# Optimization experiments

Measured on AMD Instinct MI355X. Metric: run time of the kernel, lower is better.

## Reference

```python
import jax, jax.numpy as jnp
import numpy as np

KS = 3  # kernel_size
NH, HD = 16, 64
EPS = 1e-5

# fixed offset grid v: [27, 3], meshgrid 'ij' of [-1,0,1]
_offs = np.arange(-(KS // 2), KS // 2 + 1)
V_GRID = jnp.asarray(np.stack(np.meshgrid(_offs, _offs, _offs, indexing='ij'), -1).reshape(KS ** 3, 3), dtype=jnp.float32)


def setup_inputs() -> dict:
    key = jax.random.key(0)
    ks = jax.random.split(key, 8)
    B, Cf, Cm, H, W, T = 1, 64, 64, 32, 32, 32
    C = NH * HD
    inp = {
        'F': jax.random.normal(ks[0], (B, Cf, H, W, T), jnp.float32),
        'M': jax.random.normal(ks[1], (B, Cm, H, W, T), jnp.float32),
        'gamma_f': jnp.ones((Cf,), jnp.float32),
        'beta_f': jnp.zeros((Cf,), jnp.float32),
        'w_f': jax.random.normal(ks[2], (Cf, C), jnp.float32) * 0.05,
        'b_f': jnp.zeros((C,), jnp.float32),
        'gamma_m': jnp.ones((Cm,), jnp.float32),
        'beta_m': jnp.zeros((Cm,), jnp.float32),
        'w_m': jax.random.normal(ks[3], (Cm, C), jnp.float32) * 0.05,
        'b_m': jnp.zeros((C,), jnp.float32),
        'rpb': jax.random.normal(ks[4], (NH, KS, KS, KS), jnp.float32) * 0.02,
    }
    return inp


def _pe(x, gamma, beta, w, b):
    # permute to channels-last, LayerNorm over channels, Linear proj
    x = jnp.transpose(x, (0, 2, 3, 4, 1))  # [B,H,W,T,Cin]
    mu = jnp.mean(x, axis=-1, keepdims=True)
    var = jnp.mean((x - mu) ** 2, axis=-1, keepdims=True)
    x = (x - mu) / jnp.sqrt(var + EPS) * gamma + beta
    return x @ w + b  # [B,H,W,T,C]


def _mdt_forward(F, M, gamma_f, beta_f, w_f, b_f, gamma_m, beta_m, w_m, b_m, rpb):
    scale = 1.0  # qk_scale=1
    q = _pe(F, gamma_f, beta_f, w_f, b_f)
    k = _pe(M, gamma_m, beta_m, w_m, b_m)
    B, H, W, T, C = q.shape
    nh, hd = NH, C // NH
    # [B,nh,H,W,T,hd]
    q = jnp.transpose(q.reshape(B, H, W, T, nh, hd), (0, 4, 1, 2, 3, 5)) * scale
    k = jnp.transpose(k.reshape(B, H, W, T, nh, hd), (0, 4, 1, 2, 3, 5))
    pdr = (KS - 1) // 2
    kp = jnp.pad(k, ((0, 0), (0, 0), (pdr, pdr), (pdr, pdr), (pdr, pdr), (0, 0)))
    # 3x3x3 neighborhood qk: attn [B,nh,H,W,T,27], neighbor order = dz*9+dy*3+dx (matches rpb/v flatten)
    scores = [
        jnp.einsum('bnhwtd,bnhwtd->bnhwt', q,
                   jax.lax.dynamic_slice(kp, (0, 0, dz, dy, dx, 0), (B, nh, H, W, T, hd)))
        for dz in range(KS) for dy in range(KS) for dx in range(KS)
    ]
    attn = jnp.stack(scores, axis=-1) + rpb.reshape(nh, KS ** 3)[None, :, None, None, None, :]
    attn = jax.nn.softmax(attn, axis=-1)
    x = jnp.einsum('bnhwtk,kc->bnhwtc', attn, V_GRID)  # [B,nh,H,W,T,3]
    x = jnp.transpose(x, (0, 1, 5, 2, 3, 4)).reshape(B, nh * 3, H, W, T)
    return x


def reference(F, M, gamma_f, beta_f, w_f, b_f, gamma_m, beta_m, w_m, b_m, rpb):
    return _mdt_forward(F, M, gamma_f, beta_f, w_f, b_f, gamma_m, beta_m, w_m, b_m, rpb)
```

## Files before the change

### kernel.cpp

```cpp
#include <hip/hip_runtime.h>
#include <hip/hip_bf16.h>
#include <cstdint>
#include <cstddef>

#define NVOX   32768
#define CIN    64
#define COUT   1024
#define NHEAD  16
#define HD     64
#define EPSV   1e-5f
#define MT     128
#define ROWP   72
#define OBP    136
#define KCP    72
#define KCOLS  2304
#define SCP    28

using bf16x8 = __attribute__((ext_vector_type(8))) short;
using f32x4  = __attribute__((ext_vector_type(4))) float;

__device__ __forceinline__ float bf2f(unsigned short h) {
    union { unsigned u; float f; } x; x.u = ((unsigned)h) << 16; return x.f;
}
__device__ __forceinline__ unsigned short f2bf(float f) {
    __hip_bfloat16 h = __float2bfloat16(f);
    return *reinterpret_cast<unsigned short*>(&h);
}
__device__ __forceinline__ unsigned packbf2(float a, float b) {
    return (unsigned)f2bf(a) | ((unsigned)f2bf(b) << 16);
}
template<bool BF>
__device__ __forceinline__ float LD(const void* p, size_t i) {
    if constexpr (BF) return bf2f(((const unsigned short*)p)[i]);
    else              return ((const float*)p)[i];
}
__device__ __forceinline__ int is_bf(const void* gf) {
    return ((const unsigned*)gf)[0] == 0x3F803F80u;
}

__global__ __launch_bounds__(256) void wtrans_kernel(
    const void* __restrict__ w_f, const void* __restrict__ w_m,
    const void* __restrict__ gf,
    unsigned short* __restrict__ wTf, unsigned short* __restrict__ wTm)
{
    const int bfq = is_bf(gf);
    const int sel = blockIdx.x >> 8;
    const void* w = sel ? w_m : w_f;
    unsigned short* wT = sel ? wTm : wTf;
    const int b = blockIdx.x & 255;
    const int t = threadIdx.x;
    const int c = t & 63, nl = t >> 6;
    const int n = b * 4 + nl;
    const float v = bfq ? bf2f(((const unsigned short*)w)[(size_t)c * COUT + n])
                        : ((const float*)w)[(size_t)c * COUT + n];
    wT[(size_t)n * CIN + c] = f2bf(v);
}

template<bool BF>
__device__ __forceinline__ void proj_body(
    const void* __restrict__ X,
    const void* __restrict__ gamma,
    const void* __restrict__ beta,
    const unsigned short* __restrict__ wT,
    const void* __restrict__ bias,
    unsigned short* __restrict__ out,
    char* smem)
{
    unsigned short* xnT = (unsigned short*)smem;
    unsigned short* ob  = (unsigned short*)(smem + 18432);
    float* bl           = (float*)(smem + 18432 + 17408);

    const int tid = threadIdx.x;
    const int vbase = blockIdx.x * MT;
    const int jbase = blockIdx.y * 128;
    const int wv = tid >> 6;
    const int lane = tid & 63;
    const int mm = lane & 15;
    const int quad = lane >> 4;

    if (tid < 128) bl[tid] = LD<BF>(bias, jbase + tid);

    bf16x8 bfrag[2][2];
    #pragma unroll
    for (int nt = 0; nt < 2; ++nt) {
        const int jg = jbase + wv * 32 + nt * 16 + mm;
        #pragma unroll
        for (int s = 0; s < 2; ++s)
            bfrag[nt][s] = *reinterpret_cast<const bf16x8*>(wT + (size_t)jg * CIN + s * 32 + quad * 8);
    }

    {
        const int v = tid >> 1, hf = tid & 1;
        float vals[32];
        #pragma unroll
        for (int c = 0; c < 32; ++c)
            vals[c] = LD<BF>(X, (size_t)(hf * 32 + c) * NVOX + vbase + v);
        float s = 0.f;
        #pragma unroll
        for (int c = 0; c < 32; ++c) s += vals[c];
        s += __shfl_xor(s, 1);
        const float mu = s * (1.f / 64.f);
        float var = 0.f;
        #pragma unroll
        for (int c = 0; c < 32; ++c) { const float d = vals[c] - mu; var += d * d; }
        var += __shfl_xor(var, 1);
        const float rs = rsqrtf(var * (1.f / 64.f) + EPSV);
        unsigned pk[16];
        #pragma unroll
        for (int c2 = 0; c2 < 16; ++c2) {
            const int c = hf * 32 + c2 * 2;
            const float g0 = LD<BF>(gamma, c),     b0 = LD<BF>(beta, c);
            const float g1 = LD<BF>(gamma, c + 1), b1 = LD<BF>(beta, c + 1);
            const float a  = (vals[c2 * 2]     - mu) * rs * g0 + b0;
            const float b2 = (vals[c2 * 2 + 1] - mu) * rs * g1 + b1;
            pk[c2] = packbf2(a, b2);
        }
        unsigned* dst = reinterpret_cast<unsigned*>(&xnT[v * ROWP + hf * 32]);
        #pragma unroll
        for (int j = 0; j < 4; ++j) {
            uint4 u; u.x = pk[j*4]; u.y = pk[j*4+1]; u.z = pk[j*4+2]; u.w = pk[j*4+3];
            *reinterpret_cast<uint4*>(dst + j * 4) = u;
        }
    }
    __syncthreads();

    const int headbase = blockIdx.y * 2;

    #pragma unroll
    for (int half = 0; half < 2; ++half) {
        f32x4 acc[4][2];
        #pragma unroll
        for (int mt = 0; mt < 4; ++mt)
            #pragma unroll
            for (int nt = 0; nt < 2; ++nt)
                #pragma unroll
                for (int r = 0; r < 4; ++r) acc[mt][nt][r] = 0.f;

        #pragma unroll
        for (int mt = 0; mt < 4; ++mt) {
            const unsigned short* ap = &xnT[((half * 4 + mt) * 16 + mm) * ROWP + quad * 8];
            const bf16x8 a0 = *reinterpret_cast<const bf16x8*>(ap);
            const bf16x8 a1 = *reinterpret_cast<const bf16x8*>(ap + 32);
            #pragma unroll
            for (int nt = 0; nt < 2; ++nt) {
                acc[mt][nt] = __builtin_amdgcn_mfma_f32_16x16x32_bf16(a0, bfrag[nt][0], acc[mt][nt], 0, 0, 0);
                acc[mt][nt] = __builtin_amdgcn_mfma_f32_16x16x32_bf16(a1, bfrag[nt][1], acc[mt][nt], 0, 0, 0);
            }
        }

        if (half == 1) __syncthreads();

        #pragma unroll
        for (int nt = 0; nt < 2; ++nt) {
            const int jl = wv * 32 + nt * 16 + mm;
            const float bj = bl[jl];
            #pragma unroll
            for (int mt = 0; mt < 4; ++mt)
                #pragma unroll
                for (int r = 0; r < 4; ++r)
                    ob[(mt * 16 + quad * 4 + r) * OBP + jl] = f2bf(acc[mt][nt][r] + bj);
        }
        __syncthreads();

        #pragma unroll
        for (int it = 0; it < 4; ++it) {
            const int lin = it * 256 + tid;
            const int vox = lin >> 4, c = lin & 15;
            const int hsel = c >> 3, dpart = (c & 7) * 8;
            const uint4 val = *reinterpret_cast<const uint4*>(&ob[vox * OBP + c * 8]);
            *reinterpret_cast<uint4*>(
                &out[(size_t)(headbase + hsel) * NVOX * HD
                     + (size_t)(vbase + half * 64 + vox) * HD + dpart]) = val;
        }
    }
}

__global__ __launch_bounds__(256) void proj_kernel(
    const void* F, const void* M,
    const void* gf, const void* bef, const void* gm, const void* bem,
    const unsigned short* wTf, const unsigned short* wTm,
    const void* bias_f, const void* bias_m,
    unsigned short* q, unsigned short* k)
{
    extern __shared__ char smem[];
    const int bfq = is_bf(gf);
    const int sel = blockIdx.z;
    const void* X      = sel ? M : F;
    const void* gamma  = sel ? gm : gf;
    const void* beta   = sel ? bem : bef;
    const unsigned short* wT = sel ? wTm : wTf;
    const void* bias   = sel ? bias_m : bias_f;
    unsigned short* out = sel ? k : q;
    if (bfq) proj_body<true>(X, gamma, beta, wT, bias, out, smem);
    else     proj_body<false>(X, gamma, beta, wT, bias, out, smem);
}
#define PROJ_LDS (18432 + 17408 + 512)

__global__ __launch_bounds__(256) void attn_kernel(
    const unsigned short* __restrict__ qb,
    const unsigned short* __restrict__ kb,
    const void* __restrict__ rpb,
    const void* __restrict__ gf,
    void* __restrict__ outv)
{
    __shared__ unsigned short khalo[6 * KCOLS];
    __shared__ _Float16 sc[4 * 32 * SCP];
    __shared__ float rpbl[27];

    const int bfq = is_bf(gf);
    const int tid = threadIdx.x;
    const int id = blockIdx.x + (blockIdx.y << 8);
    const int head = ((id & 7) << 1) | (id >> 11);
    const int pos = (id >> 3) & 255;
    const int wg = pos & 7, h = pos >> 3;
    const int wv = tid >> 6, lane = tid & 63;
    const int mm = lane & 15, quad = lane >> 4;
    const int w = wg * 4 + wv;

    if (tid < 27)
        rpbl[tid] = bfq ? bf2f(((const unsigned short*)rpb)[head * 27 + tid])
                        : ((const float*)rpb)[head * 27 + tid];
    {
        uint4 z; z.x = 0u; z.y = 0u; z.z = 0u; z.w = 0u;
        uint4* scv = reinterpret_cast<uint4*>(sc);
        scv[tid] = z;
        if (tid < 192) scv[256 + tid] = z;
    }

    const unsigned short* qcol = qb + ((size_t)head * NVOX + (size_t)(h * 32 + w) * 32) * HD;
    bf16x8 afr[3][2];
    #pragma unroll
    for (int s = 0; s < 3; ++s) {
        const int trow = (s == 2) ? (8 + mm) : (s * 16 + mm);
        #pragma unroll
        for (int kk = 0; kk < 2; ++kk)
            afr[s][kk] = *reinterpret_cast<const bf16x8*>(qcol + trow * HD + kk * 32 + quad * 8);
    }

    const size_t kbase = (size_t)head * NVOX * HD;
    _Float16* scw = sc + wv * (32 * SCP);

    for (int dz = 0; dz < 3; ++dz) {
        const int hh = h + dz - 1;
        const int t = tid >> 3, cs = tid & 7;
        #pragma unroll
        for (int col = 0; col < 6; ++col) {
            const int ww = wg * 4 - 1 + col;
            uint4 val; val.x = 0u; val.y = 0u; val.z = 0u; val.w = 0u;
            if ((unsigned)hh < 32u && (unsigned)ww < 32u)
                val = *reinterpret_cast<const uint4*>(
                    &kb[kbase + (size_t)((hh * 32 + ww) * 32 + t) * HD + cs * 8]);
            *reinterpret_cast<uint4*>(&khalo[col * KCOLS + t * KCP + cs * 8]) = val;
        }
        __syncthreads();

        #pragma unroll
        for (int dy = 0; dy < 3; ++dy) {
            const unsigned short* kc = &khalo[(wv + dy) * KCOLS];
            const int nbb = (dz * 3 + dy) * 3;
            #pragma unroll
            for (int sa = 0; sa < 2; ++sa) {
                bf16x8 b0 = *reinterpret_cast<const bf16x8*>(kc + (sa * 16 + mm) * KCP + quad * 8);
                bf16x8 b1 = *reinterpret_cast<const bf16x8*>(kc + (sa * 16 + mm) * KCP + 32 + quad * 8);
                f32x4 acc;
                acc[0] = 0.f; acc[1] = 0.f; acc[2] = 0.f; acc[3] = 0.f;
                acc = __builtin_amdgcn_mfma_f32_16x16x32_bf16(afr[sa][0], b0, acc, 0, 0, 0);
                acc = __builtin_amdgcn_mfma_f32_16x16x32_bf16(afr[sa][1], b1, acc, 0, 0, 0);
                #pragma unroll
                for (int r = 0; r < 4; ++r) {
                    const int tt = sa * 16 + quad * 4 + r;
                    const int dx = sa * 16 + mm - tt + 1;
                    if ((unsigned)dx < 3u)
                        scw[tt * SCP + nbb + dx] = (_Float16)acc[r];
                }
            }
            {
                bf16x8 b0 = *reinterpret_cast<const bf16x8*>(kc + (8 + mm) * KCP + quad * 8);
                bf16x8 b1 = *reinterpret_cast<const bf16x8*>(kc + (8 + mm) * KCP + 32 + quad * 8);
                f32x4 acc;
                acc[0] = 0.f; acc[1] = 0.f; acc[2] = 0.f; acc[3] = 0.f;
                acc = __builtin_amdgcn_mfma_f32_16x16x32_bf16(afr[2][0], b0, acc, 0, 0, 0);
                acc = __builtin_amdgcn_mfma_f32_16x16x32_bf16(afr[2][1], b1, acc, 0, 0, 0);
                if (quad == 1 && mm == 8)
                    scw[15 * SCP + nbb + 2] = (_Float16)acc[3];
                else if (quad == 2 && mm == 7)
                    scw[16 * SCP + nbb + 0] = (_Float16)acc[0];
            }
        }
        __syncthreads();
    }

    if (tid < 128) {
        const int wl = tid >> 5, t = tid & 31;
        const _Float16* sv = sc + wl * (32 * SCP) + t * SCP;
        float s[27];
        float mx = -1e30f;
        #pragma unroll
        for (int nb = 0; nb < 27; ++nb) {
            s[nb] = (float)sv[nb] + rpbl[nb];
            mx = fmaxf(mx, s[nb]);
        }
        float se = 0.f, s0 = 0.f, s1 = 0.f, s2 = 0.f;
        #pragma unroll
        for (int nb = 0; nb < 27; ++nb) {
            const float e = __expf(s[nb] - mx);
            se += e;
            s0 += e * (float)(nb / 9 - 1);
            s1 += e * (float)((nb / 3) % 3 - 1);
            s2 += e * (float)(nb % 3 - 1);
        }
        const float inv = 1.0f / se;
        const int gvox = (h * 32 + wg * 4 + wl) * 32 + t;
        const size_t o0 = (size_t)(head * 3 + 0) * NVOX + gvox;
        const size_t o1 = (size_t)(head * 3 + 1) * NVOX + gvox;
        const size_t o2 = (size_t)(head * 3 + 2) * NVOX + gvox;
        if (bfq) {
            unsigned short* out = (unsigned short*)outv;
            out[o0] = f2bf(s0 * inv);
            out[o1] = f2bf(s1 * inv);
            out[o2] = f2bf(s2 * inv);
        } else {
            float* out = (float*)outv;
            out[o0] = s0 * inv;
            out[o1] = s1 * inv;
            out[o2] = s2 * inv;
        }
    }
}

extern "C" void kernel_launch(void* const* d_in, const int* in_sizes, int n_in,
                              void* d_out, int out_size, void* d_ws, size_t ws_size,
                              hipStream_t stream) {
    const void* F       = d_in[0];
    const void* M       = d_in[1];
    const void* gamma_f = d_in[2];
    const void* beta_f  = d_in[3];
    const void* w_f     = d_in[4];
    const void* b_f     = d_in[5];
    const void* gamma_m = d_in[6];
    const void* beta_m  = d_in[7];
    const void* w_m     = d_in[8];
    const void* b_m     = d_in[9];
    const void* rpb     = d_in[10];

    unsigned short* q = (unsigned short*)d_ws;
    unsigned short* k = q + (size_t)NVOX * COUT;
    const size_t wt_off = 2 * (size_t)NVOX * COUT * sizeof(unsigned short);
    unsigned short* wTf;
    if (ws_size >= wt_off + 2 * (size_t)COUT * CIN * sizeof(unsigned short)) {
        wTf = (unsigned short*)((char*)d_ws + wt_off);
    } else {
        wTf = (unsigned short*)d_out;
    }
    unsigned short* wTm = wTf + (size_t)COUT * CIN;

    wtrans_kernel<<<dim3(512), dim3(256), 0, stream>>>(w_f, w_m, gamma_f, wTf, wTm);
    proj_kernel<<<dim3(NVOX / MT, COUT / 128, 2), dim3(256), PROJ_LDS, stream>>>(
        F, M, gamma_f, beta_f, gamma_m, beta_m, wTf, wTm, b_f, b_m, q, k);
    attn_kernel<<<dim3(256, NHEAD), dim3(256), 0, stream>>>(q, k, rpb, gamma_f, d_out);
}
```

Before: 175.5 us.

## Fuse neighborhood softmax into MFMA epilogue using cross-lane shuffles instead of LDS scores

Drops the LDS score buffer and the separate softmax pass done by half the threads. Each lane now pulls its three dx-neighbor scores out of the MFMA accumulator with register selects and lane shuffles, exponentiates them, and keeps running sums for the weighted offset. Only diagonal lanes write the outputs. This removes LDS stores and reads, their zero-init and a serial 27-element loop. The cost is that softmax no longer subtracts the max, so exponentials can overflow if scores are large, and the edge handling between the tiles relies on the patch shuffles being correct.

```diff
diff --git a/kernel.cpp b/kernel.cpp
--- a/kernel.cpp
+++ b/kernel.cpp
@@ -14,7 +14,6 @@
 #define OBP    136
 #define KCP    72
 #define KCOLS  2304
-#define SCP    28
 
 using bf16x8 = __attribute__((ext_vector_type(8))) short;
 using f32x4  = __attribute__((ext_vector_type(4))) float;
@@ -36,6 +35,11 @@
 }
 __device__ __forceinline__ int is_bf(const void* gf) {
     return ((const unsigned*)gf)[0] == 0x3F803F80u;
+}
+__device__ __forceinline__ float sel4(const f32x4& a, int r) {
+    const float c01 = (r & 1) ? a[1] : a[0];
+    const float c23 = (r & 1) ? a[3] : a[2];
+    return (r & 2) ? c23 : c01;
 }
 
 __global__ __launch_bounds__(256) void wtrans_kernel(
@@ -204,7 +208,6 @@
     void* __restrict__ outv)
 {
     __shared__ unsigned short khalo[6 * KCOLS];
-    __shared__ _Float16 sc[4 * 32 * SCP];
     __shared__ float rpbl[27];
 
     const int bfq = is_bf(gf);
@@ -220,12 +223,6 @@
     if (tid < 27)
         rpbl[tid] = bfq ? bf2f(((const unsigned short*)rpb)[head * 27 + tid])
                         : ((const float*)rpb)[head * 27 + tid];
-    {
-        uint4 z; z.x = 0u; z.y = 0u; z.z = 0u; z.w = 0u;
-        uint4* scv = reinterpret_cast<uint4*>(sc);
-        scv[tid] = z;
-        if (tid < 192) scv[256 + tid] = z;
-    }
 
     const unsigned short* qcol = qb + ((size_t)head * NVOX + (size_t)(h * 32 + w) * 32) * HD;
     bf16x8 afr[3][2];
@@ -238,19 +235,25 @@
     }
 
     const size_t kbase = (size_t)head * NVOX * HD;
-    _Float16* scw = sc + wv * (32 * SCP);
-
+    const int selr  = mm & 3;
+    const int selrU = (mm + 1) & 3;
+    const int selrD = (mm + 3) & 3;
+
+    float se[2] = {0.f, 0.f}, sv0[2] = {0.f, 0.f},
+          sv1[2] = {0.f, 0.f}, sv2[2] = {0.f, 0.f};
+
+    #pragma unroll
     for (int dz = 0; dz < 3; ++dz) {
         const int hh = h + dz - 1;
-        const int t = tid >> 3, cs = tid & 7;
+        const int kt = tid >> 3, cs = tid & 7;
         #pragma unroll
         for (int col = 0; col < 6; ++col) {
             const int ww = wg * 4 - 1 + col;
             uint4 val; val.x = 0u; val.y = 0u; val.z = 0u; val.w = 0u;
             if ((unsigned)hh < 32u && (unsigned)ww < 32u)
                 val = *reinterpret_cast<const uint4*>(
-                    &kb[kbase + (size_t)((hh * 32 + ww) * 32 + t) * HD + cs * 8]);
-            *reinterpret_cast<uint4*>(&khalo[col * KCOLS + t * KCP + cs * 8]) = val;
+                    &kb[kbase + (size_t)((hh * 32 + ww) * 32 + kt) * HD + cs * 8]);
+            *reinterpret_cast<uint4*>(&khalo[col * KCOLS + kt * KCP + cs * 8]) = val;
         }
         __syncthreads();
 
@@ -258,72 +261,71 @@
         for (int dy = 0; dy < 3; ++dy) {
             const unsigned short* kc = &khalo[(wv + dy) * KCOLS];
             const int nbb = (dz * 3 + dy) * 3;
+            const float r0 = rpbl[nbb + 0];
+            const float r1 = rpbl[nbb + 1];
+            const float r2 = rpbl[nbb + 2];
+
+            float patchA, patchB;
+            {
+                const bf16x8 b0 = *reinterpret_cast<const bf16x8*>(kc + (8 + mm) * KCP + quad * 8);
+                const bf16x8 b1 = *reinterpret_cast<const bf16x8*>(kc + (8 + mm) * KCP + 32 + quad * 8);
+                f32x4 macc;
+                macc[0] = 0.f; macc[1] = 0.f; macc[2] = 0.f; macc[3] = 0.f;
+                macc = __builtin_amdgcn_mfma_f32_16x16x32_bf16(afr[2][0], b0, macc, 0, 0, 0);
+                macc = __builtin_amdgcn_mfma_f32_16x16x32_bf16(afr[2][1], b1, macc, 0, 0, 0);
+                patchA = __shfl(macc[3], 24);
+                patchB = __shfl(macc[0], 39);
+            }
+
             #pragma unroll
             for (int sa = 0; sa < 2; ++sa) {
-                bf16x8 b0 = *reinterpret_cast<const bf16x8*>(kc + (sa * 16 + mm) * KCP + quad * 8);
-                bf16x8 b1 = *reinterpret_cast<const bf16x8*>(kc + (sa * 16 + mm) * KCP + 32 + quad * 8);
+                const bf16x8 b0 = *reinterpret_cast<const bf16x8*>(kc + (sa * 16 + mm) * KCP + quad * 8);
+                const bf16x8 b1 = *reinterpret_cast<const bf16x8*>(kc + (sa * 16 + mm) * KCP + 32 + quad * 8);
                 f32x4 acc;
                 acc[0] = 0.f; acc[1] = 0.f; acc[2] = 0.f; acc[3] = 0.f;
                 acc = __builtin_amdgcn_mfma_f32_16x16x32_bf16(afr[sa][0], b0, acc, 0, 0, 0);
                 acc = __builtin_amdgcn_mfma_f32_16x16x32_bf16(afr[sa][1], b1, acc, 0, 0, 0);
-                #pragma unroll
-                for (int r = 0; r < 4; ++r) {
-                    const int tt = sa * 16 + quad * 4 + r;
-                    const int dx = sa * 16 + mm - tt + 1;
-                    if ((unsigned)dx < 3u)
-                        scw[tt * SCP + nbb + dx] = (_Float16)acc[r];
-                }
+
+                const float sU = sel4(acc, selrU);
+                const float sD = sel4(acc, selrD);
+                float aL = __shfl_up(sU, 1);
+                float aR = __shfl_down(sD, 1);
+                const float aC = sel4(acc, selr);
+                if (lane == 0)  aL = (sa == 0) ? 0.f : patchB;
+                if (lane == 63) aR = (sa == 0) ? patchA : 0.f;
+
+                const float e0 = __expf(aL + r0);
+                const float e1 = __expf(aC + r1);
+                const float e2 = __expf(aR + r2);
+                const float sub = e0 + e1 + e2;
+                se[sa]  += sub;
+                if (dz == 0) sv0[sa] -= sub; else if (dz == 2) sv0[sa] += sub;
+                if (dy == 0) sv1[sa] -= sub; else if (dy == 2) sv1[sa] += sub;
+                sv2[sa] += e2 - e0;
             }
-            {
-                bf16x8 b0 = *reinterpret_cast<const bf16x8*>(kc + (8 + mm) * KCP + quad * 8);
-                bf16x8 b1 = *reinterpret_cast<const bf16x8*>(kc + (8 + mm) * KCP + 32 + quad * 8);
-                f32x4 acc;
-                acc[0] = 0.f; acc[1] = 0.f; acc[2] = 0.f; acc[3] = 0.f;
-                acc = __builtin_amdgcn_mfma_f32_16x16x32_bf16(afr[2][0], b0, acc, 0, 0, 0);
-                acc = __builtin_amdgcn_mfma_f32_16x16x32_bf16(afr[2][1], b1, acc, 0, 0, 0);
-                if (quad == 1 && mm == 8)
-                    scw[15 * SCP + nbb + 2] = (_Float16)acc[3];
-                else if (quad == 2 && mm == 7)
-                    scw[16 * SCP + nbb + 0] = (_Float16)acc[0];
+        }
+        __syncthreads();
+    }
+
+    if ((mm >> 2) == quad) {
+        #pragma unroll
+        for (int sa = 0; sa < 2; ++sa) {
+            const float inv = 1.0f / se[sa];
+            const int gvox = (h * 32 + w) * 32 + sa * 16 + mm;
+            const size_t o0 = (size_t)(head * 3 + 0) * NVOX + gvox;
+            const size_t o1 = (size_t)(head * 3 + 1) * NVOX + gvox;
+            const size_t o2 = (size_t)(head * 3 + 2) * NVOX + gvox;
+            if (bfq) {
+                unsigned short* out = (unsigned short*)outv;
+                out[o0] = f2bf(sv0[sa] * inv);
+                out[o1] = f2bf(sv1[sa] * inv);
+                out[o2] = f2bf(sv2[sa] * inv);
+            } else {
+                float* out = (float*)outv;
+                out[o0] = sv0[sa] * inv;
+                out[o1] = sv1[sa] * inv;
+                out[o2] = sv2[sa] * inv;
             }
-        }
-        __syncthreads();
-    }
-
-    if (tid < 128) {
-        const int wl = tid >> 5, t = tid & 31;
-        const _Float16* sv = sc + wl * (32 * SCP) + t * SCP;
-        float s[27];
-        float mx = -1e30f;
-        #pragma unroll
-        for (int nb = 0; nb < 27; ++nb) {
-            s[nb] = (float)sv[nb] + rpbl[nb];
-            mx = fmaxf(mx, s[nb]);
-        }
-        float se = 0.f, s0 = 0.f, s1 = 0.f, s2 = 0.f;
-        #pragma unroll
-        for (int nb = 0; nb < 27; ++nb) {
-            const float e = __expf(s[nb] - mx);
-            se += e;
-            s0 += e * (float)(nb / 9 - 1);
-            s1 += e * (float)((nb / 3) % 3 - 1);
-            s2 += e * (float)(nb % 3 - 1);
-        }
-        const float inv = 1.0f / se;
-        const int gvox = (h * 32 + wg * 4 + wl) * 32 + t;
-        const size_t o0 = (size_t)(head * 3 + 0) * NVOX + gvox;
-        const size_t o1 = (size_t)(head * 3 + 1) * NVOX + gvox;
-        const size_t o2 = (size_t)(head * 3 + 2) * NVOX + gvox;
-        if (bfq) {
-            unsigned short* out = (unsigned short*)outv;
-            out[o0] = f2bf(s0 * inv);
-            out[o1] = f2bf(s1 * inv);
-            out[o2] = f2bf(s2 * inv);
-        } else {
-            float* out = (float*)outv;
-            out[o0] = s0 * inv;
-            out[o1] = s1 * inv;
-            out[o2] = s2 * inv;
         }
     }
 }
```

Result: slower. 187.1 us (+6.6%).
